# Performance work log

Measured on AMD Instinct MI355X. Metric: run time of the kernel, lower is better.

The kernel has to match this reference:

```python
import jax, jax.numpy as jnp
import numpy as np

N_NODES = 500000
N_EDGES = 8000000
LEN_SCALE = 20000.0


def setup_inputs() -> dict:
    key = jax.random.key(0)
    ks = jax.random.split(key, 10)
    inp = {
        'read_length': jax.random.randint(ks[0], (N_NODES,), 0, 20000, dtype=jnp.int64)
        if jax.config.read('jax_enable_x64') else jax.random.randint(ks[0], (N_NODES,), 0, 20000, dtype=jnp.int32),
        'edge_index': jax.random.randint(ks[1], (2, N_EDGES), 0, N_NODES, dtype=jnp.int32),
    }
    dims = [1, 4, 8, 16, 32]
    for i in range(4):
        fan_in, fan_out = dims[i], dims[i + 1]
        inp[f'W{i+1}'] = jax.random.normal(ks[2 + 2 * i], (fan_in, fan_out), jnp.float32) / np.sqrt(fan_in)
        inp[f'b{i+1}'] = jax.random.normal(ks[3 + 2 * i], (fan_out,), jnp.float32) * 0.01
    return inp


def _gcn_conv(x, W, b, src, dst, norm_e, dinv):
    # PyG GCNConv: linear first, then D^-1/2 (A+I) D^-1/2 aggregation, then bias.
    xw = x @ W                                              # [N, F_out]
    msg = xw[src] * norm_e[:, None]                         # [E, F_out]
    agg = jax.ops.segment_sum(msg, dst, num_segments=x.shape[0])
    # self-loop term handled analytically: norm for (i,i) is deg_i^-1
    return agg + xw * dinv[:, None] + b


def reference(read_length, edge_index, W1, b1, W2, b2, W3, b3, W4, b4):
    src, dst = edge_index[0], edge_index[1]
    # x = read_length / 20000, unsqueezed to [N, 1]
    x = (read_length.astype(jnp.float32) / LEN_SCALE)[:, None]
    N = x.shape[0]
    # degree with self-loops (edge weight 1)
    deg = jax.ops.segment_sum(jnp.ones_like(src, dtype=jnp.float32), dst, num_segments=N) + 1.0
    dinv_sqrt = jax.lax.rsqrt(deg)
    dinv = 1.0 / deg
    norm_e = dinv_sqrt[src] * dinv_sqrt[dst]                # [E]
    x = _gcn_conv(x, W1, b1, src, dst, norm_e, dinv)
    x = _gcn_conv(x, W2, b2, src, dst, norm_e, dinv)
    x = _gcn_conv(x, W3, b3, src, dst, norm_e, dinv)
    x = _gcn_conv(x, W4, b4, src, dst, norm_e, dinv)
    return x
```

## Files before the change

### kernel.cpp

```cpp
#include <hip/hip_runtime.h>
#include <hip/hip_bf16.h>


#define BLK  256
#define SBLK 1024
#define NB   512
#define BSH  10
#define PB   512
#define BUFCAP 15872
#define BUF2 18176

__global__ void probe_i64(const int* __restrict__ rl32, int* __restrict__ flag) {
    int acc = 0;
    for (int k = threadIdx.x; k < 1024; k += blockDim.x)
        acc |= rl32[2 * k + 1];
    if (acc != 0) atomicOr(flag, 1);
}

__global__ __launch_bounds__(SBLK)
void bucket_count(const int* __restrict__ dst, int* __restrict__ table, int E) {
    __shared__ int h[NB];
    int j = blockIdx.x, t = threadIdx.x;
    for (int b = t; b < NB; b += SBLK) h[b] = 0;
    __syncthreads();
    int chunk = (E + PB - 1) / PB;
    int beg = j * chunk, end = min(beg + chunk, E);
    for (int e = beg + t; e < end; e += SBLK)
        atomicAdd(&h[((unsigned)dst[e]) >> BSH], 1);
    __syncthreads();
    for (int b = t; b < NB; b += SBLK) table[j * NB + b] = h[b];
}

__global__ void bucket_tot(const int* __restrict__ table, int* __restrict__ tot) {
    __shared__ int sm[BLK];
    int b = blockIdx.x, t = threadIdx.x;
    int s = 0;
    for (int j = t; j < PB; j += BLK) s += table[j * NB + b];
    sm[t] = s; __syncthreads();
    for (int off = BLK / 2; off > 0; off >>= 1) {
        if (t < off) sm[t] += sm[t + off];
        __syncthreads();
    }
    if (t == 0) tot[b] = sm[0];
}

__global__ void scan_base(const int* __restrict__ tot, int* __restrict__ base) {
    __shared__ int sm[BLK];
    int t = threadIdx.x;
    int loc[NB / BLK]; int s = 0;
#pragma unroll
    for (int k = 0; k < NB / BLK; ++k) { loc[k] = tot[t * (NB / BLK) + k]; s += loc[k]; }
    sm[t] = s; __syncthreads();
    int v = s;
    for (int off = 1; off < BLK; off <<= 1) {
        int add = (t >= off) ? sm[t - off] : 0;
        __syncthreads(); sm[t] += add; __syncthreads();
    }
    int run = sm[t] - v;
#pragma unroll
    for (int k = 0; k < NB / BLK; ++k) { base[t * (NB / BLK) + k] = run; run += loc[k]; }
    if (t == BLK - 1) base[NB] = run;
}

__global__ __launch_bounds__(64)
void scan_table(int* __restrict__ table, const int* __restrict__ base) {
    int b = blockIdx.x, lane = threadIdx.x;
    int v[PB / 64]; int s = 0;
#pragma unroll
    for (int k = 0; k < PB / 64; ++k) {
        v[k] = table[(lane * (PB / 64) + k) * NB + b];
        s += v[k];
    }
    int run = s;
    for (int off = 1; off < 64; off <<= 1) {
        int u = __shfl_up(run, off);
        if (lane >= off) run += u;
    }
    run -= s;
    run += base[b];
#pragma unroll
    for (int k = 0; k < PB / 64; ++k) {
        int t = v[k];
        table[(lane * (PB / 64) + k) * NB + b] = run;
        run += t;
    }
}

__global__ __launch_bounds__(SBLK)
void scatter(const int* __restrict__ src, const int* __restrict__ dst,
             const int* __restrict__ table, unsigned* __restrict__ epart, int E) {
    __shared__ unsigned buf[BUFCAP];
    __shared__ int h[NB];
    __shared__ int cur[NB];
    __shared__ int rbase[NB];
    int j = blockIdx.x, t = threadIdx.x;
    for (int b = t; b < NB; b += SBLK) rbase[b] = table[j * NB + b];
    int chunk = (E + PB - 1) / PB;
    int beg = j * chunk, end = min(beg + chunk, E);
    for (int s = beg; s < end; s += BUFCAP) {
        int se = min(s + BUFCAP, end);
        for (int b = t; b < NB; b += SBLK) h[b] = 0;
        __syncthreads();
        for (int e = s + t; e < se; e += SBLK)
            atomicAdd(&h[((unsigned)dst[e]) >> BSH], 1);
        __syncthreads();
        if (t < NB) cur[t] = h[t];
        __syncthreads();
        for (int off = 1; off < NB; off <<= 1) {
            int add = 0;
            if (t < NB && t >= off) add = cur[t - off];
            __syncthreads();
            if (t < NB) cur[t] += add;
            __syncthreads();
        }
        if (t < NB) cur[t] -= h[t];
        __syncthreads();
        for (int e = s + t; e < se; e += SBLK) {
            unsigned d = (unsigned)dst[e];
            int b = d >> BSH;
            int slot = atomicAdd(&cur[b], 1);
            buf[slot] = ((d & 1023u) << 19) | (unsigned)src[e];
        }
        __syncthreads();
        int w = t >> 6, lane = t & 63;
        for (int b = w; b < NB; b += (SBLK >> 6)) {
            int n = h[b];
            int lo = cur[b] - n;
            int gb = rbase[b];
            for (int k = lane; k < n; k += 64)
                epart[gb + k] = buf[lo + k];
        }
        __syncthreads();
        if (t < NB) rbase[t] += h[t];
        __syncthreads();
    }
}

__global__ __launch_bounds__(1024)
void csr_build(const unsigned* __restrict__ epart, const int* __restrict__ base,
               unsigned* __restrict__ epart2, int* __restrict__ rowp) {
    __shared__ unsigned buf[BUF2];
    __shared__ int sc[1024];
    __shared__ int cur[1024];
    int b = blockIdx.x, t = threadIdx.x;
    int beg = base[b], end = base[b + 1];
    int n = end - beg;
    sc[t] = 0;
    __syncthreads();
    for (int e = beg + t; e < end; e += 1024)
        atomicAdd(&sc[epart[e] >> 19], 1);
    __syncthreads();
    int v = sc[t];
    for (int off = 1; off < 1024; off <<= 1) {
        int add = (t >= off) ? sc[t - off] : 0;
        __syncthreads(); sc[t] += add; __syncthreads();
    }
    int start = sc[t] - v;
    rowp[b * 1024 + t] = beg + start;
    if (t == 1023) rowp[b * 1024 + 1024] = end;
    cur[t] = start;
    __syncthreads();
    if (n <= BUF2) {
        for (int e = beg + t; e < end; e += 1024) {
            unsigned p = epart[e];
            int slot = atomicAdd(&cur[p >> 19], 1);
            buf[slot] = p & 0x7FFFFu;
        }
        __syncthreads();
        for (int k = t; k < n; k += 1024)
            epart2[beg + k] = buf[k];
    } else {
        for (int e = beg + t; e < end; e += 1024) {
            unsigned p = epart[e];
            int slot = atomicAdd(&cur[p >> 19], 1);
            epart2[beg + slot] = p & 0x7FFFFu;
        }
    }
}

__global__ void init_nodes(const int* __restrict__ rl, const int* __restrict__ rowp,
                           float* __restrict__ dinv, float2* __restrict__ v0,
                           const int* __restrict__ flag, int N) {
    int i = blockIdx.x * blockDim.x + threadIdx.x;
    if (i < N) {
        int v = (*flag) ? rl[i] : rl[2 * i];
        float d = (float)(rowp[i + 1] - rowp[i]) + 1.0f;
        dinv[i] = 1.0f / d;
        float rs = rsqrtf(d);
        float2 u; u.x = rs * ((float)v * (1.0f / 20000.0f)); u.y = rs;
        v0[i] = u;
    }
}

__global__ void coeffs(const float* __restrict__ W1, const float* __restrict__ b1,
                       const float* __restrict__ W2, const float* __restrict__ b2,
                       const float* __restrict__ W3, const float* __restrict__ b3,
                       const float* __restrict__ W4, const float* __restrict__ b4,
                       float* __restrict__ c) {
    __shared__ float p3[16], q3[16], r3[16];
    int t = threadIdx.x;
    if (t == 0) {
        float p2[8], q2[8];
        for (int j = 0; j < 8; ++j) {
            float s1 = 0.f, s2 = 0.f;
            for (int k = 0; k < 4; ++k) {
                float w = W2[k * 8 + j];
                s1 += W1[k] * w;
                s2 += b1[k] * w;
            }
            p2[j] = s1; q2[j] = s2;
        }
        for (int m = 0; m < 16; ++m) {
            float s1 = 0.f, s2 = 0.f, s3 = 0.f;
            for (int j = 0; j < 8; ++j) {
                float w = W3[j * 16 + m];
                s1 += p2[j] * w; s2 += q2[j] * w;
                s3 += b2[j] * w;
            }
            p3[m] = s1; q3[m] = s2; r3[m] = s3;
        }
    }
    __syncthreads();
    if (t < 32) {
        float c4 = 0.f, c3 = 0.f, c2 = 0.f, c1 = 0.f;
        for (int k = 0; k < 16; ++k) {
            float w = W4[k * 32 + t];
            c4 += p3[k] * w; c3 += q3[k] * w; c2 += r3[k] * w;
            c1 += b3[k] * w;
        }
        c[t] = c4; c[32 + t] = c3; c[64 + t] = c2; c[96 + t] = c1;
    }
}

__global__ void gather_csr(const unsigned* __restrict__ epart2, const int* __restrict__ rowp,
                           const float2* __restrict__ vin, float2* __restrict__ vout,
                           const float* __restrict__ dinv, float* __restrict__ zsave, int N) {
    int t = blockIdx.x * blockDim.x + threadIdx.x;
    int i = t >> 3, l = t & 7;
    if (i >= N) return;
    int beg = rowp[i], end = rowp[i + 1];
    float a = 0.f, b = 0.f;
    int j = beg + l;
    for (; j + 8 < end; j += 16) {
        int s0 = (int)__builtin_nontemporal_load(&epart2[j]);
        int s1 = (int)__builtin_nontemporal_load(&epart2[j + 8]);
        float2 u0 = vin[s0];
        float2 u1 = vin[s1];
        a += u0.x + u1.x; b += u0.y + u1.y;
    }
    if (j < end) {
        int s = (int)__builtin_nontemporal_load(&epart2[j]);
        float2 u = vin[s];
        a += u.x; b += u.y;
    }
    a += __shfl_xor(a, 1); b += __shfl_xor(b, 1);
    a += __shfl_xor(a, 2); b += __shfl_xor(b, 2);
    a += __shfl_xor(a, 4); b += __shfl_xor(b, 4);
    if (l == 0) {
        float2 self = vin[i];
        float di = dinv[i];
        float2 o; o.x = (a + self.x) * di; o.y = (b + self.y) * di;
        vout[i] = o;
        if (zsave) zsave[i] = o.y;
    }
}

__global__ void write_out(const float2* __restrict__ v0, const float* __restrict__ z1,
                          const float* __restrict__ z2, const float* __restrict__ z3,
                          const float* __restrict__ dinv, const float* __restrict__ c,
                          const float* __restrict__ b4,
                          float* __restrict__ out, int N) {
    int t = blockIdx.x * blockDim.x + threadIdx.x;
    int i = t >> 5, f = t & 31;
    if (i < N) {
        float sq = rsqrtf(dinv[i]);
        float v = sq * (v0[i].x * c[f] + z3[i] * c[32 + f] + z2[i] * c[64 + f]
                        + z1[i] * c[96 + f])
                  + b4[f];
        out[(size_t)i * 32 + f] = v;
    }
}

extern "C" void kernel_launch(void* const* d_in, const int* in_sizes, int n_in,
                              void* d_out, int out_size, void* d_ws, size_t ws_size,
                              hipStream_t stream) {
    const int N = in_sizes[0];
    const int E = in_sizes[1] / 2;
    const int* rl  = (const int*)d_in[0];
    const int* src = (const int*)d_in[1];
    const int* dst = src + E;
    const float* W1 = (const float*)d_in[2];
    const float* b1 = (const float*)d_in[3];
    const float* W2 = (const float*)d_in[4];
    const float* b2 = (const float*)d_in[5];
    const float* W3 = (const float*)d_in[6];
    const float* b3 = (const float*)d_in[7];
    const float* W4 = (const float*)d_in[8];
    const float* b4 = (const float*)d_in[9];

    const int gbNode = (N + 1023) / 1024;
    const int rowpN  = gbNode * 1024 + 1;

    float*  dinv = (float*)d_ws;
    float2* v0   = (float2*)(dinv + N);
    float2* v1   = v0 + N;
    float*  z1   = (float*)(v1 + N);
    float*  z2   = z1 + N;
    float*  z3   = z2 + N;
    int*    table = (int*)(z3 + N);
    int*    rowp  = table + PB * NB;
    int*    btot  = rowp + rowpN + 3;
    int*    bbase = btot + NB;
    float*  c     = (float*)(bbase + NB + 1);
    int*    flag  = (int*)(c + 128);

    unsigned* epart  = (unsigned*)d_out;
    unsigned* epart2 = epart + E;

    hipMemsetAsync(flag, 0, sizeof(int), stream);
    probe_i64<<<1, BLK, 0, stream>>>(rl, flag);

    bucket_count<<<PB, SBLK, 0, stream>>>(dst, table, E);
    bucket_tot<<<NB, BLK, 0, stream>>>(table, btot);
    scan_base<<<1, BLK, 0, stream>>>(btot, bbase);
    scan_table<<<NB, 64, 0, stream>>>(table, bbase);
    scatter<<<PB, SBLK, 0, stream>>>(src, dst, table, epart, E);

    csr_build<<<gbNode, 1024, 0, stream>>>(epart, bbase, epart2, rowp);

    init_nodes<<<(N + BLK - 1) / BLK, BLK, 0, stream>>>(rl, rowp, dinv, v0, flag, N);
    coeffs<<<1, 64, 0, stream>>>(W1, b1, W2, b2, W3, b3, W4, b4, c);

    const int gbG = (8 * N + BLK - 1) / BLK;
    gather_csr<<<gbG, BLK, 0, stream>>>(epart2, rowp, v0, v1, dinv, z1, N);
    gather_csr<<<gbG, BLK, 0, stream>>>(epart2, rowp, v1, v0, dinv, z2, N);
    gather_csr<<<gbG, BLK, 0, stream>>>(epart2, rowp, v0, v1, dinv, z3, N);
    gather_csr<<<gbG, BLK, 0, stream>>>(epart2, rowp, v1, v0, dinv, (float*)nullptr, N);

    write_out<<<(N * 32 + BLK - 1) / BLK, BLK, 0, stream>>>(
        v0, z1, z2, z3, dinv, c, b4, (float*)d_out, N);
}
```

Baseline: 473.7 us.

## Fuse last gather with output write and trim small launches

Fuses the fourth aggregation pass with the output projection into a single gather_out kernel that writes float4 outputs, provided the CSR edge array can live in the workspace instead of the output buffer. It removes scan_base by having scan_table and csr_build compute bucket prefixes themselves, folds coeffs into an extra block of init_nodes, and replaces the memset-plus-atomic flag with a block reduction. It also drops the nontemporal hints on edge-index loads. This cuts several kernel launches and one full pass over node data, but relies on the workspace being large enough and adds redundant prefix sums per block.

```diff
diff --git a/kernel.cpp b/kernel.cpp
--- a/kernel.cpp
+++ b/kernel.cpp
@@ -11,10 +11,17 @@
 #define BUF2 18176
 
 __global__ void probe_i64(const int* __restrict__ rl32, int* __restrict__ flag) {
+    __shared__ int sm[BLK];
+    int t = threadIdx.x;
     int acc = 0;
-    for (int k = threadIdx.x; k < 1024; k += blockDim.x)
+    for (int k = t; k < 1024; k += blockDim.x)
         acc |= rl32[2 * k + 1];
-    if (acc != 0) atomicOr(flag, 1);
+    sm[t] = acc; __syncthreads();
+    for (int off = BLK / 2; off > 0; off >>= 1) {
+        if (t < off) sm[t] |= sm[t + off];
+        __syncthreads();
+    }
+    if (t == 0) *flag = (sm[0] != 0) ? 1 : 0;
 }
 
 __global__ __launch_bounds__(SBLK)
@@ -44,27 +51,13 @@
     if (t == 0) tot[b] = sm[0];
 }
 
-__global__ void scan_base(const int* __restrict__ tot, int* __restrict__ base) {
-    __shared__ int sm[BLK];
-    int t = threadIdx.x;
-    int loc[NB / BLK]; int s = 0;
-#pragma unroll
-    for (int k = 0; k < NB / BLK; ++k) { loc[k] = tot[t * (NB / BLK) + k]; s += loc[k]; }
-    sm[t] = s; __syncthreads();
-    int v = s;
-    for (int off = 1; off < BLK; off <<= 1) {
-        int add = (t >= off) ? sm[t - off] : 0;
-        __syncthreads(); sm[t] += add; __syncthreads();
-    }
-    int run = sm[t] - v;
-#pragma unroll
-    for (int k = 0; k < NB / BLK; ++k) { base[t * (NB / BLK) + k] = run; run += loc[k]; }
-    if (t == BLK - 1) base[NB] = run;
-}
-
 __global__ __launch_bounds__(64)
-void scan_table(int* __restrict__ table, const int* __restrict__ base) {
+void scan_table(int* __restrict__ table, const int* __restrict__ btot) {
     int b = blockIdx.x, lane = threadIdx.x;
+    int pre = 0;
+    for (int k = lane; k < NB; k += 64)
+        if (k < b) pre += btot[k];
+    for (int off = 1; off < 64; off <<= 1) pre += __shfl_xor(pre, off);
     int v[PB / 64]; int s = 0;
 #pragma unroll
     for (int k = 0; k < PB / 64; ++k) {
@@ -77,7 +70,7 @@
         if (lane >= off) run += u;
     }
     run -= s;
-    run += base[b];
+    run += pre;
 #pragma unroll
     for (int k = 0; k < PB / 64; ++k) {
         int t = v[k];
@@ -137,16 +130,30 @@
 }
 
 __global__ __launch_bounds__(1024)
-void csr_build(const unsigned* __restrict__ epart, const int* __restrict__ base,
+void csr_build(const unsigned* __restrict__ epart, const int* __restrict__ btot,
                unsigned* __restrict__ epart2, int* __restrict__ rowp) {
     __shared__ unsigned buf[BUF2];
     __shared__ int sc[1024];
     __shared__ int cur[1024];
+    __shared__ int s_beg, s_end;
     int b = blockIdx.x, t = threadIdx.x;
-    int beg = base[b], end = base[b + 1];
+    if (t < 64) {
+        int pre = 0, tot = 0;
+        for (int k = t; k < NB; k += 64) {
+            int v = btot[k];
+            if (k < b) pre += v;
+            if (k == b) tot = v;
+        }
+        for (int off = 1; off < 64; off <<= 1) {
+            pre += __shfl_xor(pre, off);
+            tot += __shfl_xor(tot, off);
+        }
+        if (t == 0) { s_beg = pre; s_end = pre + tot; }
+    }
+    sc[t] = 0;
+    __syncthreads();
+    int beg = s_beg, end = s_end;
     int n = end - beg;
-    sc[t] = 0;
-    __syncthreads();
     for (int e = beg + t; e < end; e += 1024)
         atomicAdd(&sc[epart[e] >> 19], 1);
     __syncthreads();
@@ -180,8 +187,49 @@
 
 __global__ void init_nodes(const int* __restrict__ rl, const int* __restrict__ rowp,
                            float* __restrict__ dinv, float2* __restrict__ v0,
-                           const int* __restrict__ flag, int N) {
-    int i = blockIdx.x * blockDim.x + threadIdx.x;
+                           const int* __restrict__ flag, int N,
+                           const float* __restrict__ W1, const float* __restrict__ b1,
+                           const float* __restrict__ W2, const float* __restrict__ b2,
+                           const float* __restrict__ W3, const float* __restrict__ b3,
+                           const float* __restrict__ W4, const float* __restrict__ b4,
+                           float* __restrict__ c) {
+    __shared__ float p3[16], q3[16], r3[16];
+    int t = threadIdx.x;
+    if (blockIdx.x == gridDim.x - 1) {
+        if (t == 0) {
+            float p2[8], q2[8];
+            for (int j = 0; j < 8; ++j) {
+                float s1 = 0.f, s2 = 0.f;
+                for (int k = 0; k < 4; ++k) {
+                    float w = W2[k * 8 + j];
+                    s1 += W1[k] * w;
+                    s2 += b1[k] * w;
+                }
+                p2[j] = s1; q2[j] = s2;
+            }
+            for (int m = 0; m < 16; ++m) {
+                float s1 = 0.f, s2 = 0.f, s3 = 0.f;
+                for (int j = 0; j < 8; ++j) {
+                    float w = W3[j * 16 + m];
+                    s1 += p2[j] * w; s2 += q2[j] * w;
+                    s3 += b2[j] * w;
+                }
+                p3[m] = s1; q3[m] = s2; r3[m] = s3;
+            }
+        }
+        __syncthreads();
+        if (t < 32) {
+            float c4 = 0.f, c3 = 0.f, c2 = 0.f, c1 = 0.f;
+            for (int k = 0; k < 16; ++k) {
+                float w = W4[k * 32 + t];
+                c4 += p3[k] * w; c3 += q3[k] * w; c2 += r3[k] * w;
+                c1 += b3[k] * w;
+            }
+            c[t] = c4; c[32 + t] = c3; c[64 + t] = c2; c[96 + t] = c1;
+        }
+        return;
+    }
+    int i = blockIdx.x * blockDim.x + t;
     if (i < N) {
         int v = (*flag) ? rl[i] : rl[2 * i];
         float d = (float)(rowp[i + 1] - rowp[i]) + 1.0f;
@@ -189,46 +237,6 @@
         float rs = rsqrtf(d);
         float2 u; u.x = rs * ((float)v * (1.0f / 20000.0f)); u.y = rs;
         v0[i] = u;
-    }
-}
-
-__global__ void coeffs(const float* __restrict__ W1, const float* __restrict__ b1,
-                       const float* __restrict__ W2, const float* __restrict__ b2,
-                       const float* __restrict__ W3, const float* __restrict__ b3,
-                       const float* __restrict__ W4, const float* __restrict__ b4,
-                       float* __restrict__ c) {
-    __shared__ float p3[16], q3[16], r3[16];
-    int t = threadIdx.x;
-    if (t == 0) {
-        float p2[8], q2[8];
-        for (int j = 0; j < 8; ++j) {
-            float s1 = 0.f, s2 = 0.f;
-            for (int k = 0; k < 4; ++k) {
-                float w = W2[k * 8 + j];
-                s1 += W1[k] * w;
-                s2 += b1[k] * w;
-            }
-            p2[j] = s1; q2[j] = s2;
-        }
-        for (int m = 0; m < 16; ++m) {
-            float s1 = 0.f, s2 = 0.f, s3 = 0.f;
-            for (int j = 0; j < 8; ++j) {
-                float w = W3[j * 16 + m];
-                s1 += p2[j] * w; s2 += q2[j] * w;
-                s3 += b2[j] * w;
-            }
-            p3[m] = s1; q3[m] = s2; r3[m] = s3;
-        }
-    }
-    __syncthreads();
-    if (t < 32) {
-        float c4 = 0.f, c3 = 0.f, c2 = 0.f, c1 = 0.f;
-        for (int k = 0; k < 16; ++k) {
-            float w = W4[k * 32 + t];
-            c4 += p3[k] * w; c3 += q3[k] * w; c2 += r3[k] * w;
-            c1 += b3[k] * w;
-        }
-        c[t] = c4; c[32 + t] = c3; c[64 + t] = c2; c[96 + t] = c1;
     }
 }
 
@@ -242,15 +250,14 @@
     float a = 0.f, b = 0.f;
     int j = beg + l;
     for (; j + 8 < end; j += 16) {
-        int s0 = (int)__builtin_nontemporal_load(&epart2[j]);
-        int s1 = (int)__builtin_nontemporal_load(&epart2[j + 8]);
+        int s0 = epart2[j];
+        int s1 = epart2[j + 8];
         float2 u0 = vin[s0];
         float2 u1 = vin[s1];
         a += u0.x + u1.x; b += u0.y + u1.y;
     }
     if (j < end) {
-        int s = (int)__builtin_nontemporal_load(&epart2[j]);
-        float2 u = vin[s];
+        float2 u = vin[epart2[j]];
         a += u.x; b += u.y;
     }
     a += __shfl_xor(a, 1); b += __shfl_xor(b, 1);
@@ -263,6 +270,43 @@
         vout[i] = o;
         if (zsave) zsave[i] = o.y;
     }
+}
+
+__global__ void gather_out(const unsigned* __restrict__ epart2, const int* __restrict__ rowp,
+                           const float2* __restrict__ vin, const float* __restrict__ dinv,
+                           const float* __restrict__ z1, const float* __restrict__ z2,
+                           const float* __restrict__ z3, const float* __restrict__ c,
+                           const float* __restrict__ b4, float* __restrict__ out, int N) {
+    int t = blockIdx.x * blockDim.x + threadIdx.x;
+    int i = t >> 3, l = t & 7;
+    if (i >= N) return;
+    int beg = rowp[i], end = rowp[i + 1];
+    float a = 0.f;
+    int j = beg + l;
+    for (; j + 8 < end; j += 16) {
+        int s0 = epart2[j];
+        int s1 = epart2[j + 8];
+        a += vin[s0].x + vin[s1].x;
+    }
+    if (j < end) a += vin[epart2[j]].x;
+    a += __shfl_xor(a, 1);
+    a += __shfl_xor(a, 2);
+    a += __shfl_xor(a, 4);
+    float di = dinv[i];
+    float ox = (a + vin[i].x) * di;
+    float sq = rsqrtf(di);
+    float zz1 = z1[i], zz2 = z2[i], zz3 = z3[i];
+    float4 cc4 = *(const float4*)&c[l * 4];
+    float4 cc3 = *(const float4*)&c[32 + l * 4];
+    float4 cc2 = *(const float4*)&c[64 + l * 4];
+    float4 cc1 = *(const float4*)&c[96 + l * 4];
+    float4 bb  = *(const float4*)&b4[l * 4];
+    float4 o4;
+    o4.x = sq * (ox * cc4.x + zz3 * cc3.x + zz2 * cc2.x + zz1 * cc1.x) + bb.x;
+    o4.y = sq * (ox * cc4.y + zz3 * cc3.y + zz2 * cc2.y + zz1 * cc1.y) + bb.y;
+    o4.z = sq * (ox * cc4.z + zz3 * cc3.z + zz2 * cc2.z + zz1 * cc1.z) + bb.z;
+    o4.w = sq * (ox * cc4.w + zz3 * cc3.w + zz2 * cc2.w + zz1 * cc1.w) + bb.w;
+    *(float4*)&out[(size_t)i * 32 + l * 4] = o4;
 }
 
 __global__ void write_out(const float2* __restrict__ v0, const float* __restrict__ z1,
@@ -301,42 +345,47 @@
     const int gbNode = (N + 1023) / 1024;
     const int rowpN  = gbNode * 1024 + 1;
 
-    float*  dinv = (float*)d_ws;
-    float2* v0   = (float2*)(dinv + N);
-    float2* v1   = v0 + N;
-    float*  z1   = (float*)(v1 + N);
-    float*  z2   = z1 + N;
-    float*  z3   = z2 + N;
-    int*    table = (int*)(z3 + N);
-    int*    rowp  = table + PB * NB;
-    int*    btot  = rowp + rowpN + 3;
-    int*    bbase = btot + NB;
-    float*  c     = (float*)(bbase + NB + 1);
-    int*    flag  = (int*)(c + 128);
-
+    char* w = (char*)d_ws;
+    float2* v0   = (float2*)w;                w += (size_t)N * 8;
+    float2* v1   = (float2*)w;                w += (size_t)N * 8;
+    float*  dinv = (float*)w;                 w += (size_t)N * 4;
+    float*  z1   = (float*)w;                 w += (size_t)N * 4;
+    float*  z2   = (float*)w;                 w += (size_t)N * 4;
+    float*  z3   = (float*)w;                 w += (size_t)N * 4;
+    int*    table = (int*)w;                  w += (size_t)PB * NB * 4;
+    int*    rowp  = (int*)w;                  w += (size_t)(rowpN + 3) * 4;
+    int*    btot  = (int*)w;                  w += NB * 4;
+    float*  c     = (float*)w;                w += 128 * 4;
+    int*    flag  = (int*)w;                  w += 16;
+    size_t used = (size_t)(w - (char*)d_ws);
+    used = (used + 255) & ~(size_t)255;
+    bool fits = (used + (size_t)E * 4) <= ws_size;
     unsigned* epart  = (unsigned*)d_out;
-    unsigned* epart2 = epart + E;
-
-    hipMemsetAsync(flag, 0, sizeof(int), stream);
+    unsigned* epart2 = fits ? (unsigned*)((char*)d_ws + used) : (epart + E);
+
     probe_i64<<<1, BLK, 0, stream>>>(rl, flag);
 
     bucket_count<<<PB, SBLK, 0, stream>>>(dst, table, E);
     bucket_tot<<<NB, BLK, 0, stream>>>(table, btot);
-    scan_base<<<1, BLK, 0, stream>>>(btot, bbase);
-    scan_table<<<NB, 64, 0, stream>>>(table, bbase);
+    scan_table<<<NB, 64, 0, stream>>>(table, btot);
     scatter<<<PB, SBLK, 0, stream>>>(src, dst, table, epart, E);
 
-    csr_build<<<gbNode, 1024, 0, stream>>>(epart, bbase, epart2, rowp);
-
-    init_nodes<<<(N + BLK - 1) / BLK, BLK, 0, stream>>>(rl, rowp, dinv, v0, flag, N);
-    coeffs<<<1, 64, 0, stream>>>(W1, b1, W2, b2, W3, b3, W4, b4, c);
+    csr_build<<<gbNode, 1024, 0, stream>>>(epart, btot, epart2, rowp);
+
+    const int nInit = (N + BLK - 1) / BLK;
+    init_nodes<<<nInit + 1, BLK, 0, stream>>>(rl, rowp, dinv, v0, flag, N,
+                                              W1, b1, W2, b2, W3, b3, W4, b4, c);
 
     const int gbG = (8 * N + BLK - 1) / BLK;
     gather_csr<<<gbG, BLK, 0, stream>>>(epart2, rowp, v0, v1, dinv, z1, N);
     gather_csr<<<gbG, BLK, 0, stream>>>(epart2, rowp, v1, v0, dinv, z2, N);
     gather_csr<<<gbG, BLK, 0, stream>>>(epart2, rowp, v0, v1, dinv, z3, N);
-    gather_csr<<<gbG, BLK, 0, stream>>>(epart2, rowp, v1, v0, dinv, (float*)nullptr, N);
-
-    write_out<<<(N * 32 + BLK - 1) / BLK, BLK, 0, stream>>>(
-        v0, z1, z2, z3, dinv, c, b4, (float*)d_out, N);
-}
+    if (fits) {
+        gather_out<<<gbG, BLK, 0, stream>>>(epart2, rowp, v1, dinv, z1, z2, z3,
+                                            c, b4, (float*)d_out, N);
+    } else {
+        gather_csr<<<gbG, BLK, 0, stream>>>(epart2, rowp, v1, v0, dinv, (float*)nullptr, N);
+        write_out<<<(N * 32 + BLK - 1) / BLK, BLK, 0, stream>>>(
+            v0, z1, z2, z3, dinv, c, b4, (float*)d_out, N);
+    }
+}
```

After: 419.2 us. 11.5% less time.
